# Kernel optimization log

Hardware: AMD Instinct MI355X
Metric: run time of the kernel (lower is better)

The kernel has to match this reference:

```python
import jax, jax.numpy as jnp
import numpy as np

EMBED_DIM = 1024
N_TOKENS = 8192


def setup_inputs() -> dict:
    key = jax.random.key(0)
    k1, k2, k3 = jax.random.split(key, 3)
    inputs = jax.random.normal(k1, (N_TOKENS, EMBED_DIM), dtype=jnp.float32)
    rotation_params = jax.random.normal(k2, (EMBED_DIM, EMBED_DIM), dtype=jnp.float32)
    entangle_params = jax.random.normal(k3, (EMBED_DIM, EMBED_DIM), dtype=jnp.float32)
    return {"inputs": inputs, "rotation_params": rotation_params, "entangle_params": entangle_params}


def reference(inputs, rotation_params, entangle_params):
    # query/key projections from externally supplied params
    embed_dim = inputs.shape[-1]
    wq = rotation_params.reshape(embed_dim, -1)
    wk = entangle_params.reshape(embed_dim, -1)
    query = inputs @ wq          # [N, d]
    key = inputs @ wk            # [N, d]
    scale = 1.0 / jnp.sqrt(jnp.float32(embed_dim))
    scores = jax.nn.softmax(jnp.einsum('nd,md->nm', query, key) * scale, axis=-1)  # [N, N]
    context = scores @ inputs    # attend over raw inputs (V = inputs)
    return context
```

## Files before the change

### kernel.cpp

```cpp
#include <hip/hip_runtime.h>
#include <hip/hip_bf16.h>


typedef _Float16 f16x8 __attribute__((ext_vector_type(8)));
typedef float    f32x4 __attribute__((ext_vector_type(4)));

__device__ __forceinline__ void g2lds16(const _Float16* g, _Float16* l) {
    __builtin_amdgcn_global_load_lds(
        (__attribute__((address_space(1))) unsigned int*)(g),
        (__attribute__((address_space(3))) unsigned int*)(l),
        16, 0, 0);
}


__global__ void prep_x(const float* __restrict__ src,
                       _Float16* __restrict__ hi, _Float16* __restrict__ lo,
                       _Float16* __restrict__ xt, int R, int C) {
    __shared__ float tile[32][33];
    int c0 = blockIdx.x * 32, r0 = blockIdx.y * 32;
    int tx = threadIdx.x, ty = threadIdx.y;
#pragma unroll
    for (int k = 0; k < 4; ++k) {
        int r = ty + 8 * k;
        size_t idx = (size_t)(r0 + r) * C + c0 + tx;
        float v = src[idx];
        tile[r][tx] = v;
        _Float16 h = (_Float16)v;
        hi[idx] = h;
        lo[idx] = (_Float16)(v - (float)h);
    }
    __syncthreads();
#pragma unroll
    for (int k = 0; k < 4; ++k) {
        float v = tile[tx][ty + 8 * k];
        xt[(size_t)(c0 + ty + 8 * k) * R + r0 + tx] = (_Float16)v;
    }
}

__global__ void transpose_split(const float* __restrict__ src,
                                _Float16* __restrict__ dhi,
                                _Float16* __restrict__ dlo,
                                int R, int C) {
    __shared__ float tile[32][33];
    int c0 = blockIdx.x * 32, r0 = blockIdx.y * 32;
    int tx = threadIdx.x, ty = threadIdx.y;
#pragma unroll
    for (int k = 0; k < 4; ++k)
        tile[ty + 8 * k][tx] = src[(size_t)(r0 + ty + 8 * k) * C + c0 + tx];
    __syncthreads();
#pragma unroll
    for (int k = 0; k < 4; ++k) {
        float v = tile[tx][ty + 8 * k];
        _Float16 h = (_Float16)v;
        size_t idx = (size_t)(c0 + ty + 8 * k) * R + r0 + tx;
        dhi[idx] = h;
        dlo[idx] = (_Float16)(v - (float)h);
    }
}

__global__ __launch_bounds__(128) void add_gran(const _Float16* __restrict__ g,
                                                float* __restrict__ out) {
    const long r = blockIdx.x;
    const int t = threadIdx.x;
    const _Float16* base = g + r * 16384 + 8192 + t * 8;
    float acc[8] = {0, 0, 0, 0, 0, 0, 0, 0};
#pragma unroll
    for (int z = 0; z < 8; ++z) {
        f16x8 v = *(const f16x8*)(base + z * 1024);
#pragma unroll
        for (int i = 0; i < 8; ++i) acc[i] += (float)v[i];
    }
    float4* o = (float4*)(out + r * 1024 + t * 8);
    o[0] = make_float4(acc[0], acc[1], acc[2], acc[3]);
    o[1] = make_float4(acc[4], acc[5], acc[6], acc[7]);
}

template <int TERMS, int BKH, int SWAP, int SPLIT_OUT, int GRAN>
__global__ __launch_bounds__(512, 2) void gemm_p4(
    const _Float16* __restrict__ Ahi, const _Float16* __restrict__ Alo,
    const _Float16* __restrict__ Bhi, const _Float16* __restrict__ Blo,
    float* __restrict__ C, _Float16* __restrict__ Chi, _Float16* __restrict__ Clo,
    long lda, long ldb, long ldc, int K, int nrb, int ncb,
    long zA, long zB, long zC) {
    static_assert(BKH == 32 || BKH == 64, "");
    constexpr int NMAT = (TERMS == 3) ? 4 : 2;
    constexpr int KK   = BKH / 32;
    constexpr int LPR  = BKH / 8;
    constexpr int MATH = 256 * BKH;
    __shared__ __align__(16) _Float16 s[2][NMAT * MATH];

    const long z = blockIdx.z;
    Ahi += z * zA; Bhi += z * zB;
    if constexpr (TERMS == 3) { Alo += z * zA; Blo += z * zB; }
    if constexpr (SPLIT_OUT) { Chi += z * zC; Clo += z * zC; }
    else if constexpr (!GRAN) C += z * zC;

    const int nb = nrb * ncb;
    const int orig = blockIdx.x;
    const int q = nb >> 3, r8 = nb & 7;
    const int xcd = orig & 7, pos = orig >> 3;
    const int sw = (xcd < r8 ? xcd * (q + 1) : r8 * (q + 1) + (xcd - r8) * q) + pos;
    int rb, cb;
    if constexpr (SWAP) { rb = sw / ncb; cb = sw % ncb; }
    else                { cb = sw / nrb; rb = sw % nrb; }
    const long rowBase = (long)rb * 256;
    const long colBase = (long)cb * 256;

    const int t = threadIdx.x;
    const int wave = t >> 6;
    const int lane = t & 63;
    const int lm = lane & 15;
    const int lq = lane >> 4;
    const int wr = wave >> 2;
    const int wc = wave & 3;
    const int wg = wave & 3;

    const int ri   = lane / LPR;
    const int slot = lane % LPR;
    const int swzW = (BKH == 32) ? ((ri >> 1) & 3) : (ri & 7);
    const int colOff = (slot ^ swzW) * 8;

    const _Float16* gB[4]; int lB[4];
    const _Float16* gA[4]; int lA[4];
#pragma unroll
    for (int b = 0; b < 4; ++b) {
        if constexpr (TERMS == 3) {
            const int rowW = (b >> 1) * 128 + wave * 16;
            const _Float16* m = (b & 1) ? Blo : Bhi;
            gB[b] = m + (colBase + rowW + ri) * ldb + colOff;
            lB[b] = (2 + (b & 1)) * MATH + rowW * BKH;
        } else {
            const int rowW = b * 64 + wave * 8;
            gB[b] = Bhi + (colBase + rowW + ri) * ldb + colOff;
            lB[b] = MATH + rowW * BKH;
        }
    }
#pragma unroll
    for (int a = 0; a < 4; ++a) {
        if constexpr (TERMS == 3) {
            const int rowW = wr * 128 + (a >> 1) * 64 + wg * 16;
            const _Float16* m = (a & 1) ? Alo : Ahi;
            gA[a] = m + (rowBase + rowW + ri) * lda + colOff;
            lA[a] = (a & 1) * MATH + rowW * BKH;
        } else {
            const int rowW = wr * 128 + a * 32 + wg * 8;
            gA[a] = Ahi + (rowBase + rowW + ri) * lda + colOff;
            lA[a] = rowW * BKH;
        }
    }

    const int swzR = (BKH == 32) ? ((lm >> 1) & 3) : (lm & 7);

    f32x4 acc[8][4];
#pragma unroll
    for (int rr = 0; rr < 8; ++rr)
#pragma unroll
        for (int cc = 0; cc < 4; ++cc)
#pragma unroll
            for (int i = 0; i < 4; ++i) acc[rr][cc][i] = 0.0f;

    const int NT = K / BKH;

#define VMW(N) asm volatile("s_waitcnt vmcnt(" #N ")" ::: "memory")
#define STB(b, buf, k0) g2lds16(gB[b] + (k0), &s[buf][lB[b]])
#define STA(a, buf, k0) g2lds16(gA[a] + (k0), &s[buf][lA[a]])

    STB(0, 0, 0); STB(1, 0, 0); STB(2, 0, 0); STB(3, 0, 0);
    STA(0, 0, 0); STA(1, 0, 0); STA(2, 0, 0); STA(3, 0, 0);
    if constexpr (TERMS == 3) { VMW(2); } else { VMW(3); }
    __builtin_amdgcn_s_barrier();

    int cur = 0;
    for (int tt = 0; tt < NT; ++tt) {
        const int nxt = cur ^ 1;
        const bool nl = (tt + 1 < NT);
        const long k1 = (long)(tt + 1) * BKH;
        const _Float16* sAh = &s[cur][0];
        const _Float16* sAl = sAh + MATH;
        const _Float16* sBh = sAh + (TERMS == 3 ? 2 : 1) * MATH;
        const _Float16* sBl = sAh + 3 * MATH;
        f16x8 bh[4 * KK], bl[TERMS == 3 ? 4 * KK : 1];
#pragma unroll
        for (int p = 0; p < 4; ++p) {
            f16x8 ah[2 * KK], al[TERMS == 3 ? 2 * KK : 1];
#pragma unroll
            for (int rr = 0; rr < 2; ++rr) {
                const int arow = wr * 128 + (2 * p + rr) * 16 + lm;
#pragma unroll
                for (int kk = 0; kk < KK; ++kk) {
                    const int off = arow * BKH + (((kk * 4 + lq) ^ swzR) << 3);
                    ah[rr * KK + kk] = *(const f16x8*)&sAh[off];
                    if constexpr (TERMS == 3)
                        al[rr * KK + kk] = *(const f16x8*)&sAl[off];
                }
            }
            if (p == 0) {
#pragma unroll
                for (int cc = 0; cc < 4; ++cc) {
                    const int brow = wc * 64 + cc * 16 + lm;
#pragma unroll
                    for (int kk = 0; kk < KK; ++kk) {
                        const int off = brow * BKH + (((kk * 4 + lq) ^ swzR) << 3);
                        bh[cc * KK + kk] = *(const f16x8*)&sBh[off];
                        if constexpr (TERMS == 3)
                            bl[cc * KK + kk] = *(const f16x8*)&sBl[off];
                    }
                }
            }
            if (nl) {
                if (p == 0)      { STB(0, nxt, k1); STB(1, nxt, k1);
                                   STB(2, nxt, k1); STB(3, nxt, k1); }
                else if (p == 1) { STA(0, nxt, k1); STA(1, nxt, k1); }
                else if (p == 2) { STA(2, nxt, k1); }
                else             { STA(3, nxt, k1); }
            }
            if constexpr (TERMS == 3) {
                if (p == 1)      { if (nl) { VMW(5); } else { VMW(0); } }
                else if (p == 3) { if (nl) { VMW(2); } }
            } else {
                if (p == 0)      { if (nl) { VMW(6); } else { VMW(2); } }
                else if (p == 1) { if (nl) { VMW(6); } else { VMW(1); } }
                else if (p == 2) { if (nl) { VMW(7); } else { VMW(0); } }
                else             { if (nl) { VMW(3); } }
            }
            __builtin_amdgcn_s_barrier();
            asm volatile("s_waitcnt lgkmcnt(0)" ::: "memory");
            __builtin_amdgcn_sched_barrier(0);
            __builtin_amdgcn_s_setprio(1);
#pragma unroll
            for (int rr = 0; rr < 2; ++rr)
#pragma unroll
                for (int cc = 0; cc < 4; ++cc)
#pragma unroll
                    for (int kk = 0; kk < KK; ++kk) {
                        acc[2 * p + rr][cc] = __builtin_amdgcn_mfma_f32_16x16x32_f16(
                            ah[rr * KK + kk], bh[cc * KK + kk], acc[2 * p + rr][cc], 0, 0, 0);
                        if constexpr (TERMS == 3) {
                            acc[2 * p + rr][cc] = __builtin_amdgcn_mfma_f32_16x16x32_f16(
                                ah[rr * KK + kk], bl[cc * KK + kk], acc[2 * p + rr][cc], 0, 0, 0);
                            acc[2 * p + rr][cc] = __builtin_amdgcn_mfma_f32_16x16x32_f16(
                                al[rr * KK + kk], bh[cc * KK + kk], acc[2 * p + rr][cc], 0, 0, 0);
                        }
                    }
            __builtin_amdgcn_s_setprio(0);
        }
        cur = nxt;
    }
#undef VMW
#undef STB
#undef STA

#pragma unroll
    for (int rr = 0; rr < 8; ++rr)
#pragma unroll
        for (int cc = 0; cc < 4; ++cc)
#pragma unroll
            for (int i = 0; i < 4; ++i) {
                const long row = rowBase + wr * 128 + rr * 16 + lq * 4 + i;
                const long col = colBase + wc * 64 + cc * 16 + lm;
                if constexpr (GRAN) {
                    Chi[row * 16384 + 8192 + z * 1024 + col] =
                        (_Float16)acc[rr][cc][i];
                } else if constexpr (SPLIT_OUT) {
                    float v = acc[rr][cc][i];
                    _Float16 h = (_Float16)v;
                    Chi[row * ldc + col] = h;
                    Clo[row * ldc + col] = (_Float16)(v - (float)h);
                } else {
                    C[row * ldc + col] = acc[rr][cc][i];
                }
            }
}

__global__ __launch_bounds__(256) void softmax_rows(const float* __restrict__ S,
                                                    _Float16* __restrict__ P,
                                                    long ldp, int N) {
    const int row = blockIdx.x;
    const int t = threadIdx.x;
    const float4* rowp = (const float4*)(S + (size_t)row * N);
    float4 v[8];
    float mx = -3.4e38f;
#pragma unroll
    for (int g = 0; g < 4; ++g) {
        v[2 * g]     = rowp[2 * t + 512 * g];
        v[2 * g + 1] = rowp[2 * t + 512 * g + 1];
    }
#pragma unroll
    for (int i = 0; i < 8; ++i)
        mx = fmaxf(mx, fmaxf(fmaxf(v[i].x, v[i].y), fmaxf(v[i].z, v[i].w)));
    __shared__ float red[8];
#pragma unroll
    for (int off = 32; off >= 1; off >>= 1) mx = fmaxf(mx, __shfl_xor(mx, off));
    if ((t & 63) == 0) red[t >> 6] = mx;
    __syncthreads();
    mx = fmaxf(fmaxf(red[0], red[1]), fmaxf(red[2], red[3]));

    float sum = 0.0f;
#pragma unroll
    for (int i = 0; i < 8; ++i) {
        v[i].x = __expf((v[i].x - mx) * 0.03125f);
        v[i].y = __expf((v[i].y - mx) * 0.03125f);
        v[i].z = __expf((v[i].z - mx) * 0.03125f);
        v[i].w = __expf((v[i].w - mx) * 0.03125f);
        sum += (v[i].x + v[i].y) + (v[i].z + v[i].w);
    }
#pragma unroll
    for (int off = 32; off >= 1; off >>= 1) sum += __shfl_xor(sum, off);
    if ((t & 63) == 0) red[4 + (t >> 6)] = sum;
    __syncthreads();
    float inv = 1.0f / (red[4] + red[5] + red[6] + red[7]);

    f16x8* prow = (f16x8*)(P + (size_t)row * ldp);
#pragma unroll
    for (int g = 0; g < 4; ++g) {
        float4 a = v[2 * g], b = v[2 * g + 1];
        f16x8 o;
        o[0] = (_Float16)(a.x * inv); o[1] = (_Float16)(a.y * inv);
        o[2] = (_Float16)(a.z * inv); o[3] = (_Float16)(a.w * inv);
        o[4] = (_Float16)(b.x * inv); o[5] = (_Float16)(b.y * inv);
        o[6] = (_Float16)(b.z * inv); o[7] = (_Float16)(b.w * inv);
        prow[t + 256 * g] = o;
    }
}

extern "C" void kernel_launch(void* const* d_in, const int* in_sizes, int n_in,
                              void* d_out, int out_size, void* d_ws, size_t ws_size,
                              hipStream_t stream) {
    const float* X  = (const float*)d_in[0];
    const float* Wq = (const float*)d_in[1];
    const float* Wk = (const float*)d_in[2];
    float* out = (float*)d_out;

    const long Nt = 8192, D = 1024;
    char* ws = (char*)d_ws;
    const size_t MB = 1024ull * 1024ull;

    _Float16* XT  = (_Float16*)(ws + 0);
    _Float16* Qhi = (_Float16*)(ws + 16 * MB);
    _Float16* Qlo = (_Float16*)(ws + 32 * MB);
    _Float16* Khi = (_Float16*)(ws + 48 * MB);
    _Float16* Klo = (_Float16*)(ws + 64 * MB);
    _Float16* Xhi   = (_Float16*)(ws + 80 * MB);
    _Float16* Xlo   = (_Float16*)(ws + 96 * MB);
    _Float16* WqThi = (_Float16*)(ws + 112 * MB);
    _Float16* WqTlo = (_Float16*)(ws + 114 * MB);
    _Float16* WkThi = (_Float16*)(ws + 116 * MB);
    _Float16* WkTlo = (_Float16*)(ws + 118 * MB);

    const size_t rowBytes = (size_t)Nt * 4;
    float* Sc = (float*)(ws + 80 * MB);
    size_t avail = ws_size > 80 * MB ? ws_size - 80 * MB : 0;
    long chunk = (long)((avail / rowBytes / 256) * 256);
    if (chunk < 256) chunk = 256;
    if (chunk > Nt) chunk = Nt;
    {
        long nch = (Nt + chunk - 1) / chunk;
        chunk = (((Nt + nch - 1) / nch) + 255) / 256 * 256;
    }

    prep_x<<<dim3(32, 256), dim3(32, 8), 0, stream>>>(X, Xhi, Xlo, XT,
                                                      (int)Nt, (int)D);
    transpose_split<<<dim3(32, 32), dim3(32, 8), 0, stream>>>(Wq, WqThi, WqTlo,
                                                              (int)D, (int)D);
    transpose_split<<<dim3(32, 32), dim3(32, 8), 0, stream>>>(Wk, WkThi, WkTlo,
                                                              (int)D, (int)D);

    gemm_p4<3, 32, 1, 1, 0><<<dim3(32 * 4, 1, 2), 512, 0, stream>>>(
        Xhi, Xlo, WqThi, WqTlo, nullptr, Qhi, Qlo,
        D, D, D, (int)D, 32, 4,
        0, (long)(4 * MB / 2), (long)(32 * MB / 2));

    long done = 0;
    while (done < Nt) {
        long cur = Nt - done < chunk ? Nt - done : chunk;
        int nrb = (int)(cur / 256), ncb = (int)(Nt / 256);
        gemm_p4<3, 32, 1, 0, 0><<<dim3(nrb * ncb, 1, 1), 512, 0, stream>>>(
            Qhi + done * D, Qlo + done * D, Khi, Klo, Sc, nullptr, nullptr,
            D, D, Nt, (int)D, nrb, ncb, 0, 0, 0);
        softmax_rows<<<(int)cur, 256, 0, stream>>>(Sc, (_Float16*)Sc,
                                                   2 * Nt, (int)Nt);
        gemm_p4<1, 64, 1, 0, 1><<<dim3(nrb * 4, 1, 8), 512, 0, stream>>>(
            (const _Float16*)Sc, nullptr, XT, nullptr,
            nullptr, (_Float16*)Sc, nullptr,
            2 * Nt, Nt, D, (int)(Nt / 8), nrb, 4,
            Nt / 8, Nt / 8, 0);
        add_gran<<<(int)cur, 128, 0, stream>>>((const _Float16*)Sc,
                                               out + done * D);
        done += cur;
    }
}
```

Before: 715.0 us.

## Switch GEMM inner product from 16x16x32 to 32x32x16 MFMA tiles

Replaces the 16x16x32 f16 MFMA fragments with 32x32x16 fragments. Each wave now holds 4x2 accumulator tiles of 16 floats instead of 8x4 tiles of 4. The LDS read pattern, the swizzle and the output index mapping are rewritten to match the new lane layout. The aim is fewer MFMA issues and fewer LDS fragment reads per FLOP through better operand reuse. The cost is different LDS bank behaviour under the changed swizzle and a different instruction latency profile.

```diff
diff --git a/kernel.cpp b/kernel.cpp
--- a/kernel.cpp
+++ b/kernel.cpp
@@ -4,6 +4,7 @@
 
 typedef _Float16 f16x8 __attribute__((ext_vector_type(8)));
 typedef float    f32x4 __attribute__((ext_vector_type(4)));
+typedef float    f32x16 __attribute__((ext_vector_type(16)));
 
 __device__ __forceinline__ void g2lds16(const _Float16* g, _Float16* l) {
     __builtin_amdgcn_global_load_lds(
@@ -84,7 +85,7 @@
     long zA, long zB, long zC) {
     static_assert(BKH == 32 || BKH == 64, "");
     constexpr int NMAT = (TERMS == 3) ? 4 : 2;
-    constexpr int KK   = BKH / 32;
+    constexpr int KK2  = BKH / 16;
     constexpr int LPR  = BKH / 8;
     constexpr int MATH = 256 * BKH;
     __shared__ __align__(16) _Float16 s[2][NMAT * MATH];
@@ -109,15 +110,15 @@
     const int t = threadIdx.x;
     const int wave = t >> 6;
     const int lane = t & 63;
-    const int lm = lane & 15;
-    const int lq = lane >> 4;
+    const int l31 = lane & 31;
+    const int lh  = lane >> 5;
     const int wr = wave >> 2;
     const int wc = wave & 3;
     const int wg = wave & 3;
 
     const int ri   = lane / LPR;
     const int slot = lane % LPR;
-    const int swzW = (BKH == 32) ? ((ri >> 1) & 3) : (ri & 7);
+    const int swzW = (BKH == 32) ? (ri & 3) : (ri & 7);
     const int colOff = (slot ^ swzW) * 8;
 
     const _Float16* gB[4]; int lB[4];
@@ -149,15 +150,15 @@
         }
     }
 
-    const int swzR = (BKH == 32) ? ((lm >> 1) & 3) : (lm & 7);
-
-    f32x4 acc[8][4];
-#pragma unroll
-    for (int rr = 0; rr < 8; ++rr)
-#pragma unroll
-        for (int cc = 0; cc < 4; ++cc)
-#pragma unroll
-            for (int i = 0; i < 4; ++i) acc[rr][cc][i] = 0.0f;
+    const int swzR = (BKH == 32) ? (lane & 3) : (lane & 7);
+
+    f32x16 acc[4][2];
+#pragma unroll
+    for (int rr = 0; rr < 4; ++rr)
+#pragma unroll
+        for (int cc = 0; cc < 2; ++cc)
+#pragma unroll
+            for (int i = 0; i < 16; ++i) acc[rr][cc][i] = 0.0f;
 
     const int NT = K / BKH;
 
@@ -179,31 +180,28 @@
         const _Float16* sAl = sAh + MATH;
         const _Float16* sBh = sAh + (TERMS == 3 ? 2 : 1) * MATH;
         const _Float16* sBl = sAh + 3 * MATH;
-        f16x8 bh[4 * KK], bl[TERMS == 3 ? 4 * KK : 1];
+        f16x8 bh[2 * KK2], bl[TERMS == 3 ? 2 * KK2 : 1];
 #pragma unroll
         for (int p = 0; p < 4; ++p) {
-            f16x8 ah[2 * KK], al[TERMS == 3 ? 2 * KK : 1];
-#pragma unroll
-            for (int rr = 0; rr < 2; ++rr) {
-                const int arow = wr * 128 + (2 * p + rr) * 16 + lm;
-#pragma unroll
-                for (int kk = 0; kk < KK; ++kk) {
-                    const int off = arow * BKH + (((kk * 4 + lq) ^ swzR) << 3);
-                    ah[rr * KK + kk] = *(const f16x8*)&sAh[off];
-                    if constexpr (TERMS == 3)
-                        al[rr * KK + kk] = *(const f16x8*)&sAl[off];
-                }
+            f16x8 ah[KK2], al[TERMS == 3 ? KK2 : 1];
+            const int arow = wr * 128 + p * 32 + l31;
+#pragma unroll
+            for (int kk = 0; kk < KK2; ++kk) {
+                const int off = arow * BKH + (((kk * 2 + lh) ^ swzR) << 3);
+                ah[kk] = *(const f16x8*)&sAh[off];
+                if constexpr (TERMS == 3)
+                    al[kk] = *(const f16x8*)&sAl[off];
             }
             if (p == 0) {
 #pragma unroll
-                for (int cc = 0; cc < 4; ++cc) {
-                    const int brow = wc * 64 + cc * 16 + lm;
-#pragma unroll
-                    for (int kk = 0; kk < KK; ++kk) {
-                        const int off = brow * BKH + (((kk * 4 + lq) ^ swzR) << 3);
-                        bh[cc * KK + kk] = *(const f16x8*)&sBh[off];
+                for (int cc = 0; cc < 2; ++cc) {
+                    const int brow = wc * 64 + cc * 32 + l31;
+#pragma unroll
+                    for (int kk = 0; kk < KK2; ++kk) {
+                        const int off = brow * BKH + (((kk * 2 + lh) ^ swzR) << 3);
+                        bh[cc * KK2 + kk] = *(const f16x8*)&sBh[off];
                         if constexpr (TERMS == 3)
-                            bl[cc * KK + kk] = *(const f16x8*)&sBl[off];
+                            bl[cc * KK2 + kk] = *(const f16x8*)&sBl[off];
                     }
                 }
             }
@@ -228,20 +226,18 @@
             __builtin_amdgcn_sched_barrier(0);
             __builtin_amdgcn_s_setprio(1);
 #pragma unroll
-            for (int rr = 0; rr < 2; ++rr)
-#pragma unroll
-                for (int cc = 0; cc < 4; ++cc)
-#pragma unroll
-                    for (int kk = 0; kk < KK; ++kk) {
-                        acc[2 * p + rr][cc] = __builtin_amdgcn_mfma_f32_16x16x32_f16(
-                            ah[rr * KK + kk], bh[cc * KK + kk], acc[2 * p + rr][cc], 0, 0, 0);
-                        if constexpr (TERMS == 3) {
-                            acc[2 * p + rr][cc] = __builtin_amdgcn_mfma_f32_16x16x32_f16(
-                                ah[rr * KK + kk], bl[cc * KK + kk], acc[2 * p + rr][cc], 0, 0, 0);
-                            acc[2 * p + rr][cc] = __builtin_amdgcn_mfma_f32_16x16x32_f16(
-                                al[rr * KK + kk], bh[cc * KK + kk], acc[2 * p + rr][cc], 0, 0, 0);
-                        }
+            for (int cc = 0; cc < 2; ++cc)
+#pragma unroll
+                for (int kk = 0; kk < KK2; ++kk) {
+                    acc[p][cc] = __builtin_amdgcn_mfma_f32_32x32x16_f16(
+                        ah[kk], bh[cc * KK2 + kk], acc[p][cc], 0, 0, 0);
+                    if constexpr (TERMS == 3) {
+                        acc[p][cc] = __builtin_amdgcn_mfma_f32_32x32x16_f16(
+                            ah[kk], bl[cc * KK2 + kk], acc[p][cc], 0, 0, 0);
+                        acc[p][cc] = __builtin_amdgcn_mfma_f32_32x32x16_f16(
+                            al[kk], bh[cc * KK2 + kk], acc[p][cc], 0, 0, 0);
                     }
+                }
             __builtin_amdgcn_s_setprio(0);
         }
         cur = nxt;
@@ -251,13 +247,14 @@
 #undef STA
 
 #pragma unroll
-    for (int rr = 0; rr < 8; ++rr)
-#pragma unroll
-        for (int cc = 0; cc < 4; ++cc)
-#pragma unroll
-            for (int i = 0; i < 4; ++i) {
-                const long row = rowBase + wr * 128 + rr * 16 + lq * 4 + i;
-                const long col = colBase + wc * 64 + cc * 16 + lm;
+    for (int rr = 0; rr < 4; ++rr)
+#pragma unroll
+        for (int cc = 0; cc < 2; ++cc)
+#pragma unroll
+            for (int i = 0; i < 16; ++i) {
+                const long row = rowBase + wr * 128 + rr * 32 +
+                                 (i & 3) + 8 * (i >> 2) + 4 * lh;
+                const long col = colBase + wc * 64 + cc * 32 + l31;
                 if constexpr (GRAN) {
                     Chi[row * 16384 + 8192 + z * 1024 + col] =
                         (_Float16)acc[rr][cc][i];
```

Measured after the change: 799.4 us. +11.8%, slower.
